# Optimization experiments

Hardware: AMD Instinct MI355X
Metric: run time of the kernel (lower is better)

## Reference

```python
import jax, jax.numpy as jnp
import numpy as np

EPS = 1e-5

def setup_inputs() -> dict:
    key = jax.random.key(0)
    ks = jax.random.split(key, 5)
    B, L, D = 8, 2048, 1024
    scale = 0.02
    return {
        "x": jax.random.normal(ks[0], (B, L, D), dtype=jnp.float32),
        "Wk": jax.random.normal(ks[1], (D, D), dtype=jnp.float32) * scale,
        "Wkg": jax.random.normal(ks[2], (D, D), dtype=jnp.float32) * scale,
        "bkg": jnp.zeros((D,), dtype=jnp.float32),
        "Wout": jax.random.normal(ks[3], (D, D), dtype=jnp.float32) * scale,
        "num_heads": 16,
    }

def reference(x, Wk, Wkg, bkg, Wout, num_heads):
    B, L, D = x.shape
    n = num_heads
    d = D // n  # per-head dim
    k = x @ Wk.T                                   # [B, L, D]
    g = jax.nn.sigmoid(x @ Wkg.T + bkg)            # [B, L, D]
    # [B, L, n, d] -> scan over L
    k = k.reshape(B, L, n, d).transpose(1, 0, 2, 3)  # [L, B, n, d]
    g = g.reshape(B, L, n, d).transpose(1, 0, 2, 3)
    inv_sqrt_d = 1.0 / np.sqrt(d)

    def step(h, xs):
        x_t, g_t = xs
        rms = jnp.sqrt(jnp.sum(h * h, axis=-1, keepdims=True)) * inv_sqrt_d
        h_hat = h / (rms + EPS)
        h_new = h_hat * g_t + x_t
        return h_new, h_new

    h0 = jnp.zeros((B, n, d), dtype=x.dtype)
    _, o = jax.lax.scan(step, h0, (k, g))          # [L, B, n, d]
    o = o.transpose(1, 0, 2, 3).reshape(B, L, D)   # [B, L, D]
    return o @ Wout.T
```

## Files before the change

### kernel.cpp

```cpp
#include <hip/hip_runtime.h>
#include <hip/hip_bf16.h>
#include <math.h>

#define BATCH 8
#define SEQL  2048
#define DIM   1024
#define MROWS (BATCH * SEQL)

typedef _Float16 f16;
typedef _Float16 f16x8 __attribute__((ext_vector_type(8)));
typedef _Float16 f16x4 __attribute__((ext_vector_type(4)));
typedef _Float16 f16x2 __attribute__((ext_vector_type(2)));
typedef float f32x4 __attribute__((ext_vector_type(4)));

typedef const __attribute__((address_space(1))) void* gp_t;
typedef __attribute__((address_space(3))) void* lp_t;
#define GLL(src, dst) __builtin_amdgcn_global_load_lds((gp_t)(src), (lp_t)(dst), 16, 0, 0)

__global__ __launch_bounds__(256) void cvt_all(const float* __restrict__ x,
                                               const float* __restrict__ Wk,
                                               const float* __restrict__ Wkg,
                                               const float* __restrict__ Wout,
                                               f16* __restrict__ xh,
                                               f16* __restrict__ Wcat,
                                               f16* __restrict__ Wouth)
{
    int i = blockIdx.x * 256 + threadIdx.x;
    const float* src; f16* dst;
    if (i < 2097152)      { src = x;    dst = xh;             }
    else if (i < 2228224) { src = Wk;   dst = Wcat;           i -= 2097152; }
    else if (i < 2359296) { src = Wkg;  dst = Wcat + 1048576; i -= 2228224; }
    else                  { src = Wout; dst = Wouth;          i -= 2359296; }
    const float4* p = (const float4*)src + (size_t)i * 2;
    const float4 a = p[0], b = p[1];
    f16x8 v;
    v[0] = (f16)a.x; v[1] = (f16)a.y; v[2] = (f16)a.z; v[3] = (f16)a.w;
    v[4] = (f16)b.x; v[5] = (f16)b.y; v[6] = (f16)b.z; v[7] = (f16)b.w;
    *(f16x8*)(dst + (size_t)i * 8) = v;
}

template<int MODE>
__global__ __launch_bounds__(512, 2) void gemm8(const f16* __restrict__ A,
                                                const f16* __restrict__ Bw,
                                                const float* __restrict__ bias,
                                                void* __restrict__ C0,
                                                void* __restrict__ C1)
{
    constexpr int K   = 1024;
    constexpr int NTI = MODE ? 8 : 4;
    constexpr int NKT = 16;
    __shared__ f16 ldsA[256 * 64];
    __shared__ f16 ldsB[256 * 64];

    const int tid = threadIdx.x;
    const int w = tid >> 6, l = tid & 63;
    const int wm = w >> 2, wn = w & 3;
    const int lrow = l & 15;
    const int l7 = l & 7, lk = l >> 4;

    const int cpx = gridDim.x >> 3;
    const int lt  = (blockIdx.x & 7) * cpx + (blockIdx.x >> 3);
    const int bm  = (lt / NTI) * 256;
    const int bn  = (lt % NTI) * 256;

    const int srl   = tid >> 3;
    const int sg    = tid & 7;
    const int scolx = (sg ^ (srl & 7)) * 8;
    const int aR0 = (srl < 32) ? srl : (96 + srl);

    const int g0 = ((lk) ^ l7) * 8;
    const int g1 = ((4 + lk) ^ l7) * 8;

#define STAGE_AQ(tt, p)                                                                  \
    do {                                                                                 \
        const int _R = 32 * (p) + aR0;                                                   \
        GLL(A + (size_t)(bm + _R) * K + (tt) * 64 + scolx, ldsA + _R * 64 + sg * 8);     \
    } while (0)

#define STAGE_BH(tt, h)                                                                  \
    do {                                                                                 \
        const int _r0 = (h) * 128 + srl;                                                 \
        GLL(Bw + (size_t)(bn + _r0) * K + (tt) * 64 + scolx, ldsB + _r0 * 64 + sg * 8);  \
        const int _r1 = _r0 + 64;                                                        \
        GLL(Bw + (size_t)(bn + _r1) * K + (tt) * 64 + scolx, ldsB + _r1 * 64 + sg * 8);  \
    } while (0)

    f32x4 acc[8][4];
    #pragma unroll
    for (int mi = 0; mi < 8; ++mi)
        #pragma unroll
        for (int ni = 0; ni < 4; ++ni) acc[mi][ni] = (f32x4){0.f, 0.f, 0.f, 0.f};

    f16x8 bf[4][2];

#define PHASE(p, VK, STG)                                                                \
    do {                                                                                 \
        asm volatile("s_waitcnt vmcnt(" #VK ")" ::: "memory");                           \
        __builtin_amdgcn_s_barrier();                                                    \
        const int _ar = (wm * 128 + 32 * (p) + lrow) * 64;                               \
        f16x8 a00 = *(const f16x8*)(ldsA + _ar + g0);                                    \
        f16x8 a01 = *(const f16x8*)(ldsA + _ar + g1);                                    \
        f16x8 a10 = *(const f16x8*)(ldsA + _ar + 1024 + g0);                             \
        f16x8 a11 = *(const f16x8*)(ldsA + _ar + 1024 + g1);                             \
        if ((p) == 0) {                                                                  \
            _Pragma("unroll")                                                            \
            for (int ni = 0; ni < 4; ++ni) {                                             \
                const int _br = (wn * 64 + ni * 16 + lrow) * 64;                         \
                bf[ni][0] = *(const f16x8*)(ldsB + _br + g0);                            \
                bf[ni][1] = *(const f16x8*)(ldsB + _br + g1);                            \
            }                                                                            \
        }                                                                                \
        STG;                                                                             \
        asm volatile("s_waitcnt lgkmcnt(0)" ::: "memory");                               \
        __builtin_amdgcn_sched_barrier(0);                                               \
        __builtin_amdgcn_s_setprio(1);                                                   \
        _Pragma("unroll")                                                                \
        for (int ni = 0; ni < 4; ++ni) {                                                 \
            acc[2*(p)][ni]   = __builtin_amdgcn_mfma_f32_16x16x32_f16(bf[ni][0], a00, acc[2*(p)][ni], 0, 0, 0);   \
            acc[2*(p)][ni]   = __builtin_amdgcn_mfma_f32_16x16x32_f16(bf[ni][1], a01, acc[2*(p)][ni], 0, 0, 0);   \
            acc[2*(p)+1][ni] = __builtin_amdgcn_mfma_f32_16x16x32_f16(bf[ni][0], a10, acc[2*(p)+1][ni], 0, 0, 0); \
            acc[2*(p)+1][ni] = __builtin_amdgcn_mfma_f32_16x16x32_f16(bf[ni][1], a11, acc[2*(p)+1][ni], 0, 0, 0); \
        }                                                                                \
        __builtin_amdgcn_s_setprio(0);                                                   \
    } while (0)

    STAGE_BH(0, 0); STAGE_AQ(0, 0);
    STAGE_BH(0, 1); STAGE_AQ(0, 1);
    STAGE_AQ(0, 2);

    for (int t = 0; t < NKT - 1; ++t) {
        PHASE(0, 2, { STAGE_AQ(t, 3); });
        PHASE(1, 2, { STAGE_BH(t + 1, 0); STAGE_AQ(t + 1, 0); });
        PHASE(2, 4, { STAGE_BH(t + 1, 1); STAGE_AQ(t + 1, 1); });
        PHASE(3, 6, { STAGE_AQ(t + 1, 2); });
    }
    PHASE(0, 2, { STAGE_AQ(NKT - 1, 3); });
    PHASE(1, 2, {});
    PHASE(2, 1, {});
    PHASE(3, 0, {});
#undef PHASE
#undef STAGE_AQ
#undef STAGE_BH

    const int mrow  = l & 15;
    const int ncol0 = (l >> 4) * 4;
    #pragma unroll
    for (int mi = 0; mi < 8; ++mi) {
        const int m = bm + wm * 128 + mi * 16 + mrow;
        #pragma unroll
        for (int ni = 0; ni < 4; ++ni) {
            const int n0 = bn + wn * 64 + ni * 16 + ncol0;
            const f32x4 v = acc[mi][ni];
            if (MODE == 0) {
                *(f32x4*)((float*)C0 + (size_t)m * DIM + n0) = v;
            } else {
                if (n0 < DIM) {
                    f16x4 o;
                    o[0] = (f16)v[0]; o[1] = (f16)v[1]; o[2] = (f16)v[2]; o[3] = (f16)v[3];
                    *(f16x4*)((f16*)C0 + (size_t)m * DIM + n0) = o;
                } else {
                    const f32x4 bv = *(const f32x4*)(bias + (n0 - DIM));
                    f16x4 o;
                    #pragma unroll
                    for (int r = 0; r < 4; ++r)
                        o[r] = (f16)(1.f / (1.f + __expf(-(v[r] + bv[r]))));
                    *(f16x4*)((f16*)C1 + (size_t)m * DIM + (n0 - DIM)) = o;
                }
            }
        }
    }
}

template<int CTRL>
__device__ __forceinline__ float dpp_add_f(float s) {
    int t = __builtin_amdgcn_update_dpp(0, __float_as_int(s), CTRL, 0xF, 0xF, true);
    return s + __int_as_float(t);
}

__device__ __forceinline__ float sumsq4(f16x2 a, f16x2 b) {
    return __builtin_amdgcn_fdot2(a, a, __builtin_amdgcn_fdot2(b, b, 0.f, false), false);
}

#define PF 16
#define CHK 64
#define WARM 96

__global__ __launch_bounds__(64) void scan_kernel(const f16* __restrict__ Kv,
                                                  const f16* __restrict__ Gv,
                                                  f16* __restrict__ Ov)
{
    const int w = blockIdx.x & 31;
    const int c = blockIdx.x >> 5;
    const int l = threadIdx.x;

    const int tc   = c * CHK;
    const int t0   = (tc > WARM) ? (tc - WARM) : 0;
    const int warm = tc - t0;

    const size_t base = (size_t)(w >> 2) * (SEQL * DIM) + (size_t)((w & 3) * 256 + l * 4);
    size_t off = base + (size_t)t0 * DIM;

    f16x2 h01 = (f16x2){(f16)0.f, (f16)0.f};
    f16x2 h23 = (f16x2){(f16)0.f, (f16)0.f};

    f16x4 kb[PF], gb[PF];
    #pragma unroll
    for (int u = 0; u < PF; ++u) {
        kb[u] = *(const f16x4*)(Kv + off + (size_t)u * DIM);
        gb[u] = *(const f16x4*)(Gv + off + (size_t)u * DIM);
    }

    #define SCAN_STEP(kc, gc, DO_ST)                                                   \
        do {                                                                           \
            const f16x2 k01 = __builtin_shufflevector((kc), (kc), 0, 1);               \
            const f16x2 k23 = __builtin_shufflevector((kc), (kc), 2, 3);               \
            const f16x2 g01 = __builtin_shufflevector((gc), (gc), 0, 1);               \
            const f16x2 g23 = __builtin_shufflevector((gc), (gc), 2, 3);               \
            const f16x2 u01 = h01 * g01;                                               \
            const f16x2 u23 = h23 * g23;                                               \
            float s = sumsq4(h01, h23);                                                \
            s = dpp_add_f<0xB1>(s);                                                    \
            s = dpp_add_f<0x4E>(s);                                                    \
            s = dpp_add_f<0x141>(s);                                                   \
            s = dpp_add_f<0x140>(s);                                                   \
            const float inv = __builtin_amdgcn_rsqf(fmaf(s, 0.015625f, 1e-8f));        \
            const f16 ih = (f16)inv;                                                   \
            const f16x2 iv = (f16x2){ih, ih};                                          \
            h01 = u01 * iv + k01;                                                      \
            h23 = u23 * iv + k23;                                                      \
            if (DO_ST) {                                                               \
                f16x4 o;                                                               \
                o[0] = h01[0]; o[1] = h01[1]; o[2] = h23[0]; o[3] = h23[1];            \
                *(f16x4*)(Ov + off) = o;                                               \
            }                                                                          \
            off += DIM;                                                                \
        } while (0)

    for (int tb = 0; tb < warm; tb += PF) {
        #pragma unroll
        for (int u = 0; u < PF; ++u) {
            const f16x4 kc = kb[u], gc = gb[u];
            const size_t poff = off + (size_t)PF * DIM;
            kb[u] = *(const f16x4*)(Kv + poff);
            gb[u] = *(const f16x4*)(Gv + poff);
            SCAN_STEP(kc, gc, 0);
        }
    }
    for (int tb = 0; tb < CHK - PF; tb += PF) {
        #pragma unroll
        for (int u = 0; u < PF; ++u) {
            const f16x4 kc = kb[u], gc = gb[u];
            const size_t poff = off + (size_t)PF * DIM;
            kb[u] = *(const f16x4*)(Kv + poff);
            gb[u] = *(const f16x4*)(Gv + poff);
            SCAN_STEP(kc, gc, 1);
        }
    }
    #pragma unroll
    for (int u = 0; u < PF; ++u) {
        const f16x4 kc = kb[u], gc = gb[u];
        SCAN_STEP(kc, gc, 1);
    }
    #undef SCAN_STEP
}

extern "C" void kernel_launch(void* const* d_in, const int* in_sizes, int n_in,
                              void* d_out, int out_size, void* d_ws, size_t ws_size,
                              hipStream_t stream) {
    const float* x    = (const float*)d_in[0];
    const float* Wk   = (const float*)d_in[1];
    const float* Wkg  = (const float*)d_in[2];
    const float* bkg  = (const float*)d_in[3];
    const float* Wout = (const float*)d_in[4];
    float* out = (float*)d_out;

    f16* xh    = (f16*)d_ws;
    f16* Kh    = xh    + (size_t)MROWS * DIM;
    f16* Gh    = Kh    + (size_t)MROWS * DIM;
    f16* Wcat  = Gh    + (size_t)MROWS * DIM;
    f16* Wouth = Wcat  + (size_t)2 * DIM * DIM;

    cvt_all<<<dim3(9728), dim3(256), 0, stream>>>(x, Wk, Wkg, Wout, xh, Wcat, Wouth);

    gemm8<1><<<dim3(512), dim3(512), 0, stream>>>(xh, Wcat, bkg, Kh, Gh);
    scan_kernel<<<dim3(1024), dim3(64), 0, stream>>>(Kh, Gh, xh);
    gemm8<0><<<dim3(256), dim3(512), 0, stream>>>(xh, Wouth, nullptr, out, nullptr);
}
```

Before: 164.9 us.

## Prefetch next phase's A fragments from LDS into double-buffered registers

Moves the LDS reads of the A operand for the next quarter-phase to right after the current phase's MFMAs, ping-ponging between two register sets (aA/aB). The vmcnt thresholds are tightened so data for the following phase has landed before the early read. The aim is to hide LDS read latency behind the barrier and the next phase's setup, so MFMAs can start sooner. In exchange it costs extra VGPRs and waits on global loads earlier, which could expose memory latency or lower occupancy.

```diff
diff --git a/kernel.cpp b/kernel.cpp
--- a/kernel.cpp
+++ b/kernel.cpp
@@ -85,6 +85,15 @@
         GLL(Bw + (size_t)(bn + _r1) * K + (tt) * 64 + scolx, ldsB + _r1 * 64 + sg * 8);  \
     } while (0)
 
+#define READ_A(q, dst)                                                                   \
+    do {                                                                                 \
+        const int _ar = (wm * 128 + 32 * (q) + lrow) * 64;                               \
+        dst[0] = *(const f16x8*)(ldsA + _ar + g0);                                       \
+        dst[1] = *(const f16x8*)(ldsA + _ar + g1);                                       \
+        dst[2] = *(const f16x8*)(ldsA + _ar + 1024 + g0);                                \
+        dst[3] = *(const f16x8*)(ldsA + _ar + 1024 + g1);                                \
+    } while (0)
+
     f32x4 acc[8][4];
     #pragma unroll
     for (int mi = 0; mi < 8; ++mi)
@@ -92,16 +101,12 @@
         for (int ni = 0; ni < 4; ++ni) acc[mi][ni] = (f32x4){0.f, 0.f, 0.f, 0.f};
 
     f16x8 bf[4][2];
-
-#define PHASE(p, VK, STG)                                                                \
+    f16x8 aA[4], aB[4];
+
+#define PHASE(p, VK, STG, AREG, RA_Q, RA_DST)                                            \
     do {                                                                                 \
         asm volatile("s_waitcnt vmcnt(" #VK ")" ::: "memory");                           \
         __builtin_amdgcn_s_barrier();                                                    \
-        const int _ar = (wm * 128 + 32 * (p) + lrow) * 64;                               \
-        f16x8 a00 = *(const f16x8*)(ldsA + _ar + g0);                                    \
-        f16x8 a01 = *(const f16x8*)(ldsA + _ar + g1);                                    \
-        f16x8 a10 = *(const f16x8*)(ldsA + _ar + 1024 + g0);                             \
-        f16x8 a11 = *(const f16x8*)(ldsA + _ar + 1024 + g1);                             \
         if ((p) == 0) {                                                                  \
             _Pragma("unroll")                                                            \
             for (int ni = 0; ni < 4; ++ni) {                                             \
@@ -116,29 +121,34 @@
         __builtin_amdgcn_s_setprio(1);                                                   \
         _Pragma("unroll")                                                                \
         for (int ni = 0; ni < 4; ++ni) {                                                 \
-            acc[2*(p)][ni]   = __builtin_amdgcn_mfma_f32_16x16x32_f16(bf[ni][0], a00, acc[2*(p)][ni], 0, 0, 0);   \
-            acc[2*(p)][ni]   = __builtin_amdgcn_mfma_f32_16x16x32_f16(bf[ni][1], a01, acc[2*(p)][ni], 0, 0, 0);   \
-            acc[2*(p)+1][ni] = __builtin_amdgcn_mfma_f32_16x16x32_f16(bf[ni][0], a10, acc[2*(p)+1][ni], 0, 0, 0); \
-            acc[2*(p)+1][ni] = __builtin_amdgcn_mfma_f32_16x16x32_f16(bf[ni][1], a11, acc[2*(p)+1][ni], 0, 0, 0); \
+            acc[2*(p)][ni]   = __builtin_amdgcn_mfma_f32_16x16x32_f16(bf[ni][0], AREG[0], acc[2*(p)][ni], 0, 0, 0);   \
+            acc[2*(p)][ni]   = __builtin_amdgcn_mfma_f32_16x16x32_f16(bf[ni][1], AREG[1], acc[2*(p)][ni], 0, 0, 0);   \
+            acc[2*(p)+1][ni] = __builtin_amdgcn_mfma_f32_16x16x32_f16(bf[ni][0], AREG[2], acc[2*(p)+1][ni], 0, 0, 0); \
+            acc[2*(p)+1][ni] = __builtin_amdgcn_mfma_f32_16x16x32_f16(bf[ni][1], AREG[3], acc[2*(p)+1][ni], 0, 0, 0); \
         }                                                                                \
         __builtin_amdgcn_s_setprio(0);                                                   \
+        if ((RA_Q) >= 0) READ_A(RA_Q, RA_DST);                                           \
     } while (0)
 
     STAGE_BH(0, 0); STAGE_AQ(0, 0);
     STAGE_BH(0, 1); STAGE_AQ(0, 1);
     STAGE_AQ(0, 2);
+    asm volatile("s_waitcnt vmcnt(4)" ::: "memory");
+    __builtin_amdgcn_s_barrier();
+    READ_A(0, aA);
 
     for (int t = 0; t < NKT - 1; ++t) {
-        PHASE(0, 2, { STAGE_AQ(t, 3); });
-        PHASE(1, 2, { STAGE_BH(t + 1, 0); STAGE_AQ(t + 1, 0); });
-        PHASE(2, 4, { STAGE_BH(t + 1, 1); STAGE_AQ(t + 1, 1); });
-        PHASE(3, 6, { STAGE_AQ(t + 1, 2); });
-    }
-    PHASE(0, 2, { STAGE_AQ(NKT - 1, 3); });
-    PHASE(1, 2, {});
-    PHASE(2, 1, {});
-    PHASE(3, 0, {});
+        PHASE(0, 1, { STAGE_AQ(t, 3); },                          aA, 1, aB);
+        PHASE(1, 1, { STAGE_BH(t + 1, 0); STAGE_AQ(t + 1, 0); },  aB, 2, aA);
+        PHASE(2, 3, { STAGE_BH(t + 1, 1); STAGE_AQ(t + 1, 1); },  aA, 3, aB);
+        PHASE(3, 3, { STAGE_AQ(t + 1, 2); },                      aB, 0, aA);
+    }
+    PHASE(0, 1, { STAGE_AQ(NKT - 1, 3); }, aA, 1, aB);
+    PHASE(1, 1, {},                        aB, 2, aA);
+    PHASE(2, 0, {},                        aA, 3, aB);
+    PHASE(3, 0, {},                        aB, -1, aA);
 #undef PHASE
+#undef READ_A
 #undef STAGE_AQ
 #undef STAGE_BH
 
```

Result: slower. 174.3 us (+5.7%).
